# Kernel tuning notes

Measured on AMD Instinct MI355X. Metric: run time of the kernel, lower is better.

Reference implementation:

```python
import jax, jax.numpy as jnp
import numpy as np

N = 204800   # total nodes (4096 subgraphs x 50 nodes)
E = 3276800  # edges (avg degree 16)
B = 4096     # number of subgraphs
IN = 64      # in_feats
HID = 32     # latent_dim per layer
CAT = 128    # 4 * 32 concatenated states
PH = 64      # pooling hidden dim
R = 3        # num_relations
NB = 2       # num_bases
MARGIN = 1.0


def setup_inputs() -> dict:
    key = jax.random.key(0)
    ks = jax.random.split(key, 24)
    s = 0.1
    inp = {}
    inp['x'] = jax.random.normal(ks[0], (N, IN), jnp.float32)
    inp['edge_norm'] = jax.random.uniform(ks[1], (E,), jnp.float32)
    inp['src'] = jax.random.randint(ks[2], (E,), 0, N, jnp.int32)
    inp['dst'] = jax.random.randint(ks[3], (E,), 0, N, jnp.int32)
    inp['etype'] = jax.random.randint(ks[4], (E,), 0, R, jnp.int32)
    inp['graph_id'] = jnp.arange(N, dtype=jnp.int32) // (N // B)
    inp['ntype'] = jax.random.randint(ks[5], (N,), 0, 2, jnp.int32)
    # layer 0: basis-decomposed RelGraphConv (in=64 -> 32)
    inp['bases0'] = jax.random.normal(ks[6], (NB, IN, HID), jnp.float32) * s
    inp['coef0'] = jax.random.normal(ks[7], (R, NB), jnp.float32)
    inp['wself0'] = jax.random.normal(ks[8], (IN, HID), jnp.float32) * s
    inp['bias0'] = jnp.zeros((HID,), jnp.float32)
    # layers 1..3 stacked (32 -> 32 each)
    inp['bases_r'] = jax.random.normal(ks[9], (3, NB, HID, HID), jnp.float32) * s
    inp['coef_r'] = jax.random.normal(ks[10], (3, R, NB), jnp.float32)
    inp['wself_r'] = jax.random.normal(ks[11], (3, HID, HID), jnp.float32) * s
    inp['bias_r'] = jnp.zeros((3, HID), jnp.float32)
    # attention pooling (user / item)
    inp['wp_u'] = jax.random.normal(ks[12], (CAT, PH), jnp.float32) * s
    inp['wt_u'] = jax.random.normal(ks[13], (CAT, PH), jnp.float32) * s
    inp['wp_i'] = jax.random.normal(ks[14], (CAT, PH), jnp.float32) * s
    inp['wt_i'] = jax.random.normal(ks[15], (CAT, PH), jnp.float32) * s
    # MLP head
    inp['w1'] = jax.random.normal(ks[16], (2 * PH, 64), jnp.float32) * s
    inp['b1'] = jnp.zeros((64,), jnp.float32)
    inp['w2'] = jax.random.normal(ks[17], (64, 1), jnp.float32) * s
    inp['b2'] = jnp.zeros((1,), jnp.float32)
    return inp


def _rgcn_layer(h, bases, coef, wself, bias, src, dst, etype, edge_norm):
    # basis decomposition: W_r = sum_b coef[r,b] * bases[b]
    W = jnp.einsum('rb,bio->rio', coef, bases)          # [R, in, out]
    xr = jnp.einsum('ni,rio->nro', h, W)                # [N, R, out] (transform then gather)
    msg = xr[src, etype] * edge_norm[:, None]           # [E, out]
    agg = jax.ops.segment_sum(msg, dst, num_segments=N) # scatter-add to dst
    return jnp.tanh(agg + h @ wself + bias)


def _attn_pool(x, mask, gid, wp, wt):
    # x: [N, CAT], mask: [N] bool (target node type), gid: [N] graph ids
    fmask = mask.astype(x.dtype)
    cnt = jax.ops.segment_sum(fmask, gid, num_segments=B)              # [B]
    tmean = jax.ops.segment_sum(x * fmask[:, None], gid, num_segments=B)
    tmean = tmean / (cnt[:, None] + 1e-8)                              # [B, CAT]
    p = x @ wp                                                          # [N, PH]
    t = tmean @ wt                                                      # [B, PH]
    score = jnp.sum(p * t[gid], axis=-1) / jnp.sqrt(jnp.float32(PH))    # [N]
    score = jnp.where(mask, score, -1e9)
    m = jax.ops.segment_max(score, gid, num_segments=B)                 # [B]
    a = jnp.exp(score - m[gid]) * fmask
    z = jax.ops.segment_sum(a, gid, num_segments=B)
    alpha = a / (z[gid] + 1e-8)
    return jax.ops.segment_sum(alpha[:, None] * p, gid, num_segments=B)  # [B, PH]


def reference(x, edge_norm, src, dst, etype, graph_id, ntype,
              bases0, coef0, wself0, bias0, bases_r, coef_r, wself_r, bias_r,
              wp_u, wt_u, wp_i, wt_i, w1, b1, w2, b2):
    h = x
    states = []
    h = _rgcn_layer(h, bases0, coef0, wself0, bias0, src, dst, etype, edge_norm)
    states.append(h)
    for l in range(3):
        h = _rgcn_layer(h, bases_r[l], coef_r[l], wself_r[l], bias_r[l],
                        src, dst, etype, edge_norm)
        states.append(h)
    hcat = jnp.concatenate(states, axis=1)  # [N, 128]

    mask_u = ntype == 0
    mask_i = ntype == 1

    # triplet contrastive loss over per-graph mean user/item embeddings
    fu = mask_u.astype(hcat.dtype)
    fi = mask_i.astype(hcat.dtype)
    cu = jax.ops.segment_sum(fu, graph_id, num_segments=B) + 1e-8
    ci = jax.ops.segment_sum(fi, graph_id, num_segments=B) + 1e-8
    au = jax.ops.segment_sum(hcat * fu[:, None], graph_id, num_segments=B) / cu[:, None]
    ai = jax.ops.segment_sum(hcat * fi[:, None], graph_id, num_segments=B) / ci[:, None]
    an = jnp.roll(ai, 1, axis=0)  # negatives from shifted graphs
    dpos = jnp.sum((au - ai) ** 2, axis=-1)
    dneg = jnp.sum((au - an) ** 2, axis=-1)
    triplet_loss = jnp.mean(jax.nn.relu(dpos - dneg + MARGIN))

    x_u = _attn_pool(hcat, mask_u, graph_id, wp_u, wt_u)  # [B, 64]
    x_i = _attn_pool(hcat, mask_i, graph_id, wp_i, wt_i)  # [B, 64]
    z = jnp.concatenate([x_u, x_i], axis=1)               # [B, 128]
    z = jax.nn.relu(z @ w1 + b1)                          # dropout off (eval)
    out = jax.nn.sigmoid(z @ w2 + b2)[:, 0]               # [B]
    return out, triplet_loss
```

## Files before the change

kernel.cpp:

```cpp
#include <hip/hip_runtime.h>
#include <cstdint>
#include <cstddef>

#define NN   204800
#define EE   3276800
#define BB   4096
#define GS   50
#define NBUCK 200
#define CHUNK 8192
#define BCAP  17408

typedef __attribute__((ext_vector_type(8))) short short8v;
typedef __attribute__((ext_vector_type(4))) float f32x4;

__device__ __forceinline__ float bf2f(unsigned short u) {
  unsigned int x = ((unsigned int)u) << 16;
  return __int_as_float((int)x);
}
__device__ __forceinline__ unsigned short f2bf(float f) {
  unsigned int x = __float_as_uint(f);
  unsigned int r = (x + 0x7fffu + ((x >> 16) & 1u)) >> 16;
  return (unsigned short)r;
}

__global__ __launch_bounds__(256) void pass1_kernel(const int* __restrict__ src,
                                                    const int* __restrict__ dst,
                                                    const int* __restrict__ etype,
                                                    const float* __restrict__ en,
                                                    int* __restrict__ gcursor,
                                                    int2* __restrict__ staging) {
  __shared__ int2 stage[CHUNK];
  __shared__ unsigned char bid[CHUNK];
  __shared__ int hist[NBUCK], cur[NBUCK], lo[NBUCK], gbase[NBUCK];
  __shared__ int sc[256];
  const int tid = threadIdx.x;
  const int ebase = blockIdx.x * CHUNK;

  for (int i = tid; i < NBUCK; i += 256) hist[i] = 0;
  __syncthreads();
  for (int i = tid; i < CHUNK; i += 256) {
    int bk = dst[ebase + i] >> 10;
    bid[i] = (unsigned char)bk;
    atomicAdd(&hist[bk], 1);
  }
  __syncthreads();
  int hv = (tid < NBUCK) ? hist[tid] : 0;
  sc[tid] = hv;
  __syncthreads();
  for (int off = 1; off < 256; off <<= 1) {
    int t = (tid >= off) ? sc[tid - off] : 0;
    __syncthreads();
    sc[tid] += t;
    __syncthreads();
  }
  if (tid < NBUCK) {
    int excl = sc[tid] - hv;
    lo[tid]  = excl;
    cur[tid] = excl;
    gbase[tid] = hv ? atomicAdd(&gcursor[tid], hv) : 0;
  }
  __syncthreads();
  for (int i = tid; i < CHUNK; i += 256) {
    int bk = bid[i];
    int p = atomicAdd(&cur[bk], 1);
    int s  = src[ebase + i];
    int et = etype[ebase + i];
    int d  = dst[ebase + i];
    int2 r;
    r.x = (s << 12) | (et << 10) | (d & 1023);
    r.y = __float_as_int(en[ebase + i]);
    stage[p] = r;
  }
  __syncthreads();
  const int wave = tid >> 6, lane = tid & 63;
  for (int bk = wave; bk < NBUCK; bk += 4) {
    const int len = hist[bk];
    const int l0  = lo[bk];
    const int gb  = gbase[bk];
    for (int i = lane; i < len; i += 64)
      staging[gb + i] = stage[l0 + i];
  }
}

__global__ __launch_bounds__(256) void pass2_kernel(const int2* __restrict__ staging,
                                                    const int* __restrict__ gcursor,
                                                    int* __restrict__ begs,
                                                    int* __restrict__ ends,
                                                    int2* __restrict__ edata) {
  __shared__ int lhist[1024];
  __shared__ int lcur[1024];
  __shared__ int psum[256];
  const int b = blockIdx.x;
  const int tid = threadIdx.x;
  const int base = b * BCAP;
  const int cnt  = gcursor[b] - base;

  for (int i = tid; i < 1024; i += 256) lhist[i] = 0;
  __syncthreads();
  for (int i = tid; i < cnt; i += 256)
    atomicAdd(&lhist[staging[base + i].x & 1023], 1);
  __syncthreads();
  int s0 = lhist[4 * tid], s1 = lhist[4 * tid + 1];
  int s2 = lhist[4 * tid + 2], s3 = lhist[4 * tid + 3];
  int tot = s0 + s1 + s2 + s3;
  psum[tid] = tot;
  __syncthreads();
  for (int off = 1; off < 256; off <<= 1) {
    int t = (tid >= off) ? psum[tid - off] : 0;
    __syncthreads();
    psum[tid] += t;
    __syncthreads();
  }
  int o0 = base + psum[tid] - tot;
  int o1 = o0 + s0, o2 = o1 + s1, o3 = o2 + s2;
  const int nodeb = b * 1024;
  begs[nodeb + 4 * tid]     = o0;  ends[nodeb + 4 * tid]     = o1;  lcur[4 * tid]     = o0;
  begs[nodeb + 4 * tid + 1] = o1;  ends[nodeb + 4 * tid + 1] = o2;  lcur[4 * tid + 1] = o1;
  begs[nodeb + 4 * tid + 2] = o2;  ends[nodeb + 4 * tid + 2] = o3;  lcur[4 * tid + 2] = o2;
  begs[nodeb + 4 * tid + 3] = o3;  ends[nodeb + 4 * tid + 3] = o3 + s3;  lcur[4 * tid + 3] = o3;
  __syncthreads();
  for (int i = tid; i < cnt; i += 256) {
    int2 r = staging[base + i];
    int pos = atomicAdd(&lcur[r.x & 1023], 1);
    int s  = r.x >> 12;
    int et = (r.x >> 10) & 3;
    int2 outr;
    outr.x = (s << 8) + (et << 6);
    outr.y = r.y;
    edata[pos] = outr;
  }
}

__global__ __launch_bounds__(256) void wprep_kernel(
    const float* __restrict__ bases0, const float* __restrict__ coef0,
    const float* __restrict__ wself0,
    const float* __restrict__ bases_r, const float* __restrict__ coef_r,
    const float* __restrict__ wself_r,
    const float* __restrict__ wp_u, const float* __restrict__ wp_i,
    const float* __restrict__ wt_u, const float* __restrict__ wt_i,
    const float* __restrict__ w1,
    float* __restrict__ Wbuf, int* __restrict__ gcursor) {
  if (blockIdx.x == 0 && threadIdx.x < NBUCK)
    gcursor[threadIdx.x] = threadIdx.x * BCAP;
  int idx = blockIdx.x * 256 + threadIdx.x;
  if (idx < 8192) {
    int i = idx >> 7, j = idx & 127;
    float v;
    if (j < 96) {
      int r = j >> 5, f = j & 31;
      v = coef0[r * 2 + 0] * bases0[0 * 2048 + i * 32 + f]
        + coef0[r * 2 + 1] * bases0[1 * 2048 + i * 32 + f];
    } else {
      v = wself0[i * 32 + (j - 96)];
    }
    Wbuf[idx] = v;
    return;
  }
  int idx2 = idx - 8192;
  if (idx2 < 3 * 4096) {
    int l = idx2 >> 12, rem = idx2 & 4095;
    int i = rem >> 7, j = rem & 127;
    float v;
    if (j < 96) {
      int r = j >> 5, f = j & 31;
      v = coef_r[l * 6 + r * 2 + 0] * bases_r[l * 2048 + 0 * 1024 + i * 32 + f]
        + coef_r[l * 6 + r * 2 + 1] * bases_r[l * 2048 + 1 * 1024 + i * 32 + f];
    } else {
      v = wself_r[l * 1024 + i * 32 + (j - 96)];
    }
    Wbuf[idx] = v;
    return;
  }
  int idx3 = idx2 - 12288;
  if (idx3 < 32768) {
    int side = idx3 >> 14;
    int r = idx3 & 16383;
    int kk = r >> 7, k = r & 127;
    const float* wp = side ? wp_i : wp_u;
    const float* wt = side ? wt_i : wt_u;
    float acc = 0.f;
#pragma unroll 8
    for (int j = 0; j < 64; ++j)
      acc = fmaf(wp[k * 64 + j], wt[kk * 64 + j], acc);
    Wbuf[idx] = acc * 0.125f;
    return;
  }
  int idx4 = idx3 - 32768;
  if (idx4 < 16384) {
    int kp = idx4 >> 6, t = idx4 & 63;
    int side = kp >> 7, k = kp & 127;
    const float* wp = side ? wp_i : wp_u;
    float acc = 0.f;
#pragma unroll 8
    for (int j = 0; j < 64; ++j)
      acc = fmaf(wp[k * 64 + j], w1[(side * 64 + j) * 64 + t], acc);
    Wbuf[idx] = acc;
  }
}

__global__ __launch_bounds__(256) void wprep2_kernel(const float* __restrict__ Wbuf,
                                                     unsigned short* __restrict__ Whi,
                                                     unsigned short* __restrict__ Wlo) {
  int e = blockIdx.x * 256 + threadIdx.x;
  if (e >= 20480) return;
  float v;
  if (e < 8192) {
    int j = e & 7, l = (e >> 3) & 63, c = (e >> 9) & 7, q = e >> 12;
    int k   = q * 32 + (l >> 4) * 8 + j;
    int col = c * 16 + (l & 15);
    v = Wbuf[k * 128 + col];
  } else {
    int e2 = e - 8192;
    int lay = e2 >> 12, r = e2 & 4095;
    int j = r & 7, l = (r >> 3) & 63, qc = r >> 9;
    int q = qc >> 1, c = qc & 1;
    int k = q * 32 + (l >> 4) * 8 + j;
    int o = c * 16 + (l & 15);
    const float* Wc = Wbuf + 8192 + lay * 4096;
    v = (k < 96) ? Wc[(k & 31) * 128 + (k >> 5) * 32 + o]
                 : Wc[(k - 96) * 128 + 96 + o];
  }
  unsigned short hi = f2bf(v);
  Whi[e] = hi;
  Wlo[e] = f2bf(v - bf2f(hi));
}

__global__ __launch_bounds__(256) void transform_l0_kernel(
    const float* __restrict__ x,
    const unsigned short* __restrict__ Whi, const unsigned short* __restrict__ Wlo,
    unsigned short* __restrict__ Tb0) {
  __shared__ float C[64][129];
  const int tid = threadIdx.x;
  const int wv = tid >> 6, l = tid & 63;
  const int l15 = l & 15, kg = l >> 4;
  const int row = blockIdx.x * 64 + wv * 16 + l15;

  short8v ah[2], al[2];
#pragma unroll
  for (int q = 0; q < 2; ++q) {
    const float* xp = x + (size_t)row * 64 + q * 32 + kg * 8;
    const float4 v0 = *reinterpret_cast<const float4*>(xp);
    const float4 v1 = *reinterpret_cast<const float4*>(xp + 4);
    const float vv[8] = {v0.x, v0.y, v0.z, v0.w, v1.x, v1.y, v1.z, v1.w};
#pragma unroll
    for (int f = 0; f < 8; ++f) {
      const unsigned short h = f2bf(vv[f]);
      ah[q][f] = (short)h;
      al[q][f] = (short)f2bf(vv[f] - bf2f(h));
    }
  }

#pragma unroll
  for (int c = 0; c < 8; ++c) {
    f32x4 a = {0.f, 0.f, 0.f, 0.f};
#pragma unroll
    for (int q = 0; q < 2; ++q) {
      const size_t fb = ((size_t)(q * 8 + c) * 64 + l) * 8;
      const short8v bh = *reinterpret_cast<const short8v*>(Whi + fb);
      const short8v bl = *reinterpret_cast<const short8v*>(Wlo + fb);
      a = __builtin_amdgcn_mfma_f32_16x16x32_bf16(ah[q], bh, a, 0, 0, 0);
      a = __builtin_amdgcn_mfma_f32_16x16x32_bf16(al[q], bh, a, 0, 0, 0);
      a = __builtin_amdgcn_mfma_f32_16x16x32_bf16(ah[q], bl, a, 0, 0, 0);
    }
#pragma unroll
    for (int r = 0; r < 4; ++r)
      C[wv * 16 + kg * 4 + r][c * 16 + l15] = a[r];
  }
  __syncthreads();

  const int row64 = tid & 63, q = tid >> 6;
  const int node = blockIdx.x * 64 + row64;
#pragma unroll
  for (int v = 0; v < 4; ++v) {
    const int cb = q * 32 + v * 8;
    uint4 pk;
    pk.x = (unsigned)f2bf(C[row64][cb + 0]) | ((unsigned)f2bf(C[row64][cb + 1]) << 16);
    pk.y = (unsigned)f2bf(C[row64][cb + 2]) | ((unsigned)f2bf(C[row64][cb + 3]) << 16);
    pk.z = (unsigned)f2bf(C[row64][cb + 4]) | ((unsigned)f2bf(C[row64][cb + 5]) << 16);
    pk.w = (unsigned)f2bf(C[row64][cb + 6]) | ((unsigned)f2bf(C[row64][cb + 7]) << 16);
    *reinterpret_cast<uint4*>(Tb0 + (size_t)node * 128 + cb) = pk;
  }
}

__global__ __launch_bounds__(256) void aggregate_l0_kernel(
    const unsigned short* __restrict__ Tb0,
    const int* __restrict__ begs, const int* __restrict__ ends,
    const int2* __restrict__ edata, const float* __restrict__ bias,
    float* __restrict__ hcat, unsigned short* __restrict__ hbA) {
  const int node = blockIdx.x * 32 + (threadIdx.x >> 3);
  const int f4   = (threadIdx.x & 7) * 4;
  const int loff = f4 * 2;
  const char* Tbc = (const char*)Tb0;
  const int beg = begs[node];
  const int end = ends[node];
  const ushort4 sb = *reinterpret_cast<const ushort4*>(Tbc + (size_t)node * 256 + 192 + loff);
  const float4 bv  = *reinterpret_cast<const float4*>(&bias[f4]);
  float ax = bf2f(sb.x) + bv.x, ay = bf2f(sb.y) + bv.y;
  float az = bf2f(sb.z) + bv.z, aw = bf2f(sb.w) + bv.w;

  int k = beg;
  for (; k + 8 <= end; k += 8) {
    int2 ed[8];
#pragma unroll
    for (int u = 0; u < 8; ++u) ed[u] = edata[k + u];
    ushort4 mv[8];
#pragma unroll
    for (int u = 0; u < 8; ++u)
      mv[u] = *reinterpret_cast<const ushort4*>(Tbc + ed[u].x + loff);
#pragma unroll
    for (int u = 0; u < 8; ++u) {
      const float nm = __int_as_float(ed[u].y);
      ax = fmaf(bf2f(mv[u].x), nm, ax);
      ay = fmaf(bf2f(mv[u].y), nm, ay);
      az = fmaf(bf2f(mv[u].z), nm, az);
      aw = fmaf(bf2f(mv[u].w), nm, aw);
    }
  }
  for (; k < end; ++k) {
    int2 e0 = edata[k];
    const float nm = __int_as_float(e0.y);
    ushort4 m0 = *reinterpret_cast<const ushort4*>(Tbc + e0.x + loff);
    ax = fmaf(bf2f(m0.x), nm, ax);
    ay = fmaf(bf2f(m0.y), nm, ay);
    az = fmaf(bf2f(m0.z), nm, az);
    aw = fmaf(bf2f(m0.w), nm, aw);
  }
  float4 o;
  o.x = tanhf(ax); o.y = tanhf(ay); o.z = tanhf(az); o.w = tanhf(aw);
  *reinterpret_cast<float4*>(&hcat[(size_t)node * 128 + f4]) = o;
  ushort4 h;
  h.x = f2bf(o.x); h.y = f2bf(o.y); h.z = f2bf(o.z); h.w = f2bf(o.w);
  *reinterpret_cast<ushort4*>(hbA + (size_t)node * 32 + f4) = h;
}

__global__ __launch_bounds__(256, 8) void agg_tf_kernel(
    const unsigned short* __restrict__ hbX,
    const int* __restrict__ begs, const int* __restrict__ ends,
    const int2* __restrict__ edata,
    const unsigned short* __restrict__ Whi, const unsigned short* __restrict__ Wlo,
    const float* __restrict__ bias,
    float* __restrict__ hcatSlot, unsigned short* __restrict__ hbY) {
  __shared__ __align__(16) unsigned short sld[32][136];
  __shared__ float C[32][33];
  const int tid = threadIdx.x;

  {
    const int nl   = tid >> 3;
    const int node = blockIdx.x * 32 + nl;
    const int f4   = (tid & 7) * 4;
    const int loff = f4 * 2;
    const char* hbc = (const char*)hbX;
    const int beg = begs[node], end = ends[node];
    float a0x = 0.f, a0y = 0.f, a0z = 0.f, a0w = 0.f;
    float a1x = 0.f, a1y = 0.f, a1z = 0.f, a1w = 0.f;
    float a2x = 0.f, a2y = 0.f, a2z = 0.f, a2w = 0.f;

    int k = beg;
    for (; k + 8 <= end; k += 8) {
      int2 ed[8];
#pragma unroll
      for (int u = 0; u < 8; ++u) ed[u] = edata[k + u];
      ushort4 mv[8];
#pragma unroll
      for (int u = 0; u < 8; ++u)
        mv[u] = *reinterpret_cast<const ushort4*>(hbc + ((ed[u].x >> 2) & ~63) + loff);
#pragma unroll
      for (int u = 0; u < 8; ++u) {
        const int et = (ed[u].x >> 6) & 3;
        const float nm = __int_as_float(ed[u].y);
        const float n0 = (et == 0) ? nm : 0.f;
        const float n1 = (et == 1) ? nm : 0.f;
        const float n2 = (et == 2) ? nm : 0.f;
        const float vx = bf2f(mv[u].x), vy = bf2f(mv[u].y);
        const float vz = bf2f(mv[u].z), vw = bf2f(mv[u].w);
        a0x = fmaf(vx, n0, a0x); a0y = fmaf(vy, n0, a0y);
        a0z = fmaf(vz, n0, a0z); a0w = fmaf(vw, n0, a0w);
        a1x = fmaf(vx, n1, a1x); a1y = fmaf(vy, n1, a1y);
        a1z = fmaf(vz, n1, a1z); a1w = fmaf(vw, n1, a1w);
        a2x = fmaf(vx, n2, a2x); a2y = fmaf(vy, n2, a2y);
        a2z = fmaf(vz, n2, a2z); a2w = fmaf(vw, n2, a2w);
      }
    }
    for (; k < end; ++k) {
      int2 e0 = edata[k];
      const int et = (e0.x >> 6) & 3;
      const float nm = __int_as_float(e0.y);
      const float n0 = (et == 0) ? nm : 0.f;
      const float n1 = (et == 1) ? nm : 0.f;
      const float n2 = (et == 2) ? nm : 0.f;
      ushort4 m0 = *reinterpret_cast<const ushort4*>(hbc + ((e0.x >> 2) & ~63) + loff);
      const float vx = bf2f(m0.x), vy = bf2f(m0.y), vz = bf2f(m0.z), vw = bf2f(m0.w);
      a0x = fmaf(vx, n0, a0x); a0y = fmaf(vy, n0, a0y);
      a0z = fmaf(vz, n0, a0z); a0w = fmaf(vw, n0, a0w);
      a1x = fmaf(vx, n1, a1x); a1y = fmaf(vy, n1, a1y);
      a1z = fmaf(vz, n1, a1z); a1w = fmaf(vw, n1, a1w);
      a2x = fmaf(vx, n2, a2x); a2y = fmaf(vy, n2, a2y);
      a2z = fmaf(vz, n2, a2z); a2w = fmaf(vw, n2, a2w);
    }
    ushort4 s0, s1, s2;
    s0.x = f2bf(a0x); s0.y = f2bf(a0y); s0.z = f2bf(a0z); s0.w = f2bf(a0w);
    s1.x = f2bf(a1x); s1.y = f2bf(a1y); s1.z = f2bf(a1z); s1.w = f2bf(a1w);
    s2.x = f2bf(a2x); s2.y = f2bf(a2y); s2.z = f2bf(a2z); s2.w = f2bf(a2w);
    *reinterpret_cast<ushort4*>(&sld[nl][f4])      = s0;
    *reinterpret_cast<ushort4*>(&sld[nl][32 + f4]) = s1;
    *reinterpret_cast<ushort4*>(&sld[nl][64 + f4]) = s2;
    *reinterpret_cast<ushort4*>(&sld[nl][96 + f4]) =
        *reinterpret_cast<const ushort4*>(hbX + (size_t)node * 32 + f4);
  }
  __syncthreads();

  {
    const int w = tid >> 6, l = tid & 63;
    const int rg = w & 1, c = w >> 1;
    const int l15 = l & 15, kg = l >> 4;
    const int row = rg * 16 + l15;
    short8v af[4];
#pragma unroll
    for (int q = 0; q < 4; ++q)
      af[q] = *reinterpret_cast<const short8v*>(&sld[row][q * 32 + kg * 8]);
    f32x4 a = {0.f, 0.f, 0.f, 0.f};
#pragma unroll
    for (int q = 0; q < 4; ++q) {
      const size_t fb = ((size_t)(q * 2 + c) * 64 + l) * 8;
      const short8v bh = *reinterpret_cast<const short8v*>(Whi + fb);
      const short8v bl = *reinterpret_cast<const short8v*>(Wlo + fb);
      a = __builtin_amdgcn_mfma_f32_16x16x32_bf16(af[q], bh, a, 0, 0, 0);
      a = __builtin_amdgcn_mfma_f32_16x16x32_bf16(af[q], bl, a, 0, 0, 0);
    }
#pragma unroll
    for (int r = 0; r < 4; ++r)
      C[rg * 16 + kg * 4 + r][c * 16 + l15] = a[r];
  }
  __syncthreads();

  {
    const int row32 = tid & 31, g = tid >> 5;
    const int node = blockIdx.x * 32 + row32;
    float z[4];
#pragma unroll
    for (int v = 0; v < 4; ++v)
      z[v] = tanhf(C[row32][g * 4 + v] + bias[g * 4 + v]);
    float4 f0 = {z[0], z[1], z[2], z[3]};
    *reinterpret_cast<float4*>(hcatSlot + (size_t)node * 128 + g * 4) = f0;
    if (hbY) {
      ushort4 pk;
      pk.x = f2bf(z[0]); pk.y = f2bf(z[1]); pk.z = f2bf(z[2]); pk.w = f2bf(z[3]);
      *reinterpret_cast<ushort4*>(hbY + (size_t)node * 32 + g * 4) = pk;
    }
  }
}

__global__ __launch_bounds__(256) void pool_head_kernel(
    const float* __restrict__ hcat, const int* __restrict__ ntype,
    const float* __restrict__ Mt,
    const float* __restrict__ W1c,
    const float* __restrict__ b1,
    const float* __restrict__ w2, const float* __restrict__ b2,
    float* __restrict__ out, float* __restrict__ tl) {
  __shared__ float hl[GS * 129];
  __shared__ float scr[1024];
  __shared__ float av2[256];
  __shared__ float red[4];
  __shared__ float cnts[4];
  __shared__ int   snt[64];
  __shared__ int   sntp[64];

  const int g    = (blockIdx.x & 7) * (BB / 8) + (blockIdx.x >> 3);
  const int gp   = (g + BB - 1) & (BB - 1);
  const int tid  = threadIdx.x;
  const int lane = tid & 63;

  const float* hg  = hcat + (size_t)g  * (GS * 128);
  const float* hp  = hcat + (size_t)gp * (GS * 128);
  const int*   ntg = ntype + g  * GS;
  const int*   ntp = ntype + gp * GS;

  if (tid < 64) {
    snt[tid] = (tid < GS) ? ntg[tid] : 99;
    unsigned long long bu = __ballot(snt[tid] == 0);
    unsigned long long bi = __ballot(snt[tid] == 1);
    if (lane == 0) {
      cnts[0] = 1.f / ((float)__popcll(bu) + 1e-8f);
      cnts[1] = 1.f / ((float)__popcll(bi) + 1e-8f);
    }
  } else if (tid < 128) {
    sntp[lane] = (lane < GS) ? ntp[lane] : 99;
    unsigned long long bp = __ballot(sntp[lane] == 1);
    if (lane == 0) cnts[2] = 1.f / ((float)__popcll(bp) + 1e-8f);
  }

  {
    const int rowg = tid >> 5;
    const int kq   = (tid & 31) * 4;
    float spx = 0.f, spy = 0.f, spz = 0.f, spw = 0.f;
#pragma unroll
    for (int p = 0; p < 7; ++p) {
      const int r = rowg + 8 * p;
      if (r < GS) {
        const float4 v = *reinterpret_cast<const float4*>(hg + r * 128 + kq);
        hl[r * 129 + kq + 0] = v.x;
        hl[r * 129 + kq + 1] = v.y;
        hl[r * 129 + kq + 2] = v.z;
        hl[r * 129 + kq + 3] = v.w;
        if (ntp[r] == 1) {
          const float4 w = *reinterpret_cast<const float4*>(hp + r * 128 + kq);
          spx += w.x; spy += w.y; spz += w.z; spw += w.w;
        }
      }
    }
    scr[rowg * 128 + kq + 0] = spx;
    scr[rowg * 128 + kq + 1] = spy;
    scr[rowg * 128 + kq + 2] = spz;
    scr[rowg * 128 + kq + 3] = spw;
  }
  __syncthreads();

  if (tid < 128) {
    const int kf = tid;
    float su = 0.f, si = 0.f;
#pragma unroll
    for (int r = 0; r < GS; ++r) {
      const float v = hl[r * 129 + kf];
      if (snt[r] == 0) su += v; else si += v;
    }
    float sp = 0.f;
#pragma unroll
    for (int rg = 0; rg < 8; ++rg) sp += scr[rg * 128 + kf];
    const float auk = su * cnts[0];
    const float aik = si * cnts[1];
    const float apk = sp * cnts[2];
    av2[kf]       = auk;
    av2[128 + kf] = aik;
    float d1 = (auk - aik) * (auk - aik);
    float d2 = (auk - apk) * (auk - apk);
    for (int o = 32; o; o >>= 1) {
      d1 += __shfl_xor(d1, o);
      d2 += __shfl_xor(d2, o);
    }
    if (lane == 0) { red[tid >> 6] = d1; red[2 + (tid >> 6)] = d2; }
  }
  __syncthreads();

  {
    const int side = tid >> 7, kf = tid & 127;
    const float* M  = Mt + (size_t)side * 16384 + kf;
    const float* av = av2 + side * 128;
    float a0 = 0.f, a1 = 0.f, a2 = 0.f, a3 = 0.f;
#pragma unroll 4
    for (int kk = 0; kk < 128; kk += 4) {
      a0 = fmaf(M[(kk + 0) * 128], av[kk + 0], a0);
      a1 = fmaf(M[(kk + 1) * 128], av[kk + 1], a1);
      a2 = fmaf(M[(kk + 2) * 128], av[kk + 2], a2);
      a3 = fmaf(M[(kk + 3) * 128], av[kk + 3], a3);
    }
    scr[tid] = (a0 + a1) + (a2 + a3);
  }
  if (tid == 0) tl[g] = fmaxf(0.f, (red[0] + red[1]) - (red[2] + red[3]) + 1.0f);
  __syncthreads();

  if (tid < 128) {
    const int side = tid >> 6;
    const float* q = scr + side * 128;
    float v = -1e9f;
    bool msk = false;
    if (lane < GS) {
      msk = (snt[lane] == side);
      float a0 = 0.f, a1 = 0.f;
#pragma unroll 8
      for (int k = 0; k < 128; k += 2) {
        a0 = fmaf(hl[lane * 129 + k], q[k], a0);
        a1 = fmaf(hl[lane * 129 + k + 1], q[k + 1], a1);
      }
      v = msk ? (a0 + a1) : -1e9f;
    }
    float m = v;
    for (int o = 32; o; o >>= 1) m = fmaxf(m, __shfl_xor(m, o));
    float e = (lane < GS && msk) ? expf(v - m) : 0.f;
    float z = e;
    for (int o = 32; o; o >>= 1) z += __shfl_xor(z, o);
    const float invz = 1.f / (z + 1e-8f);
    if (lane < GS) scr[256 + side * 64 + lane] = e * invz;
  }
  __syncthreads();

  {
    const int side = tid >> 7, kf = tid & 127;
    const float* a = scr + 256 + side * 64;
    float acc = 0.f;
#pragma unroll
    for (int nl = 0; nl < GS; ++nl)
      acc = fmaf(a[nl], hl[nl * 129 + kf], acc);
    scr[384 + side * 128 + kf] = acc;
  }
  __syncthreads();

  {
    const int j = tid & 63, c = tid >> 6;
    const float* Wc = W1c + (size_t)c * 64 * 64 + j;
    const float* cv = scr + 384 + c * 64;
    float a0 = 0.f, a1 = 0.f, a2 = 0.f, a3 = 0.f;
#pragma unroll 4
    for (int k = 0; k < 64; k += 4) {
      a0 = fmaf(Wc[(k + 0) * 64], cv[k + 0], a0);
      a1 = fmaf(Wc[(k + 1) * 64], cv[k + 1], a1);
      a2 = fmaf(Wc[(k + 2) * 64], cv[k + 2], a2);
      a3 = fmaf(Wc[(k + 3) * 64], cv[k + 3], a3);
    }
    scr[640 + c * 64 + j] = (a0 + a1) + (a2 + a3);
  }
  __syncthreads();

  if (tid < 64) {
    const float z1 = fmaxf(b1[tid] + scr[640 + tid] + scr[704 + tid] +
                           scr[768 + tid] + scr[832 + tid], 0.f);
    float p = z1 * w2[tid];
    for (int o = 32; o; o >>= 1) p += __shfl_xor(p, o);
    if (tid == 0) out[g] = 1.f / (1.f + expf(-(p + b2[0])));
  }
}

__global__ __launch_bounds__(256) void tl_reduce_kernel(const float* __restrict__ tl,
                                                        float* __restrict__ out) {
  __shared__ float s[256];
  float acc = 0.f;
  for (int i = threadIdx.x; i < BB; i += 256) acc += tl[i];
  s[threadIdx.x] = acc;
  __syncthreads();
  for (int off = 128; off > 0; off >>= 1) {
    if (threadIdx.x < off) s[threadIdx.x] += s[threadIdx.x + off];
    __syncthreads();
  }
  if (threadIdx.x == 0) out[BB] = s[0] * (1.f / (float)BB);
}

extern "C" void kernel_launch(void* const* d_in, const int* in_sizes, int n_in,
                              void* d_out, int out_size, void* d_ws, size_t ws_size,
                              hipStream_t stream) {
  const float* x        = (const float*)d_in[0];
  const float* edge_nrm = (const float*)d_in[1];
  const int*   src      = (const int*)d_in[2];
  const int*   dst      = (const int*)d_in[3];
  const int*   etype    = (const int*)d_in[4];
  const int*   ntype    = (const int*)d_in[6];
  const float* bases0   = (const float*)d_in[7];
  const float* coef0    = (const float*)d_in[8];
  const float* wself0   = (const float*)d_in[9];
  const float* bias0    = (const float*)d_in[10];
  const float* bases_r  = (const float*)d_in[11];
  const float* coef_r   = (const float*)d_in[12];
  const float* wself_r  = (const float*)d_in[13];
  const float* bias_r   = (const float*)d_in[14];
  const float* wp_u     = (const float*)d_in[15];
  const float* wt_u     = (const float*)d_in[16];
  const float* wp_i     = (const float*)d_in[17];
  const float* wt_i     = (const float*)d_in[18];
  const float* w1       = (const float*)d_in[19];
  const float* b1       = (const float*)d_in[20];
  const float* w2       = (const float*)d_in[21];
  const float* b2       = (const float*)d_in[22];
  float* out = (float*)d_out;

  float*          hcat = (float*)d_ws;
  float*          R    = hcat + (size_t)NN * 128;
  int2*           staging = (int2*)R;
  unsigned short* Tb0  = (unsigned short*)R;
  unsigned short* hbA  = Tb0 + (size_t)NN * 128;
  unsigned short* hbB  = hbA + (size_t)NN * 32;
  int2*  edata   = (int2*)(R + (size_t)NN * 128);
  int*   begs    = (int*)(edata + (size_t)NBUCK * BCAP);
  int*   ends    = begs + NN;
  int*   gcursor = ends + NN;
  float* Wbuf    = (float*)(gcursor + 256);
  unsigned short* Whi = (unsigned short*)(Wbuf + 69632);
  unsigned short* Wlo = Whi + 20480;
  float* tl      = Wbuf + 69632 + 10240;

  size_t need = ((size_t)NN * 128 * 2 + (size_t)NBUCK * BCAP * 2 + 2 * NN + 256 +
                 69632 + 10240 + BB) * 4;
  if (ws_size < need) return;

  wprep_kernel<<<(69632 + 255) / 256, 256, 0, stream>>>(
      bases0, coef0, wself0, bases_r, coef_r, wself_r,
      wp_u, wp_i, wt_u, wt_i, w1, Wbuf, gcursor);
  wprep2_kernel<<<80, 256, 0, stream>>>(Wbuf, Whi, Wlo);

  pass1_kernel<<<EE / CHUNK, 256, 0, stream>>>(src, dst, etype, edge_nrm,
                                               gcursor, staging);
  pass2_kernel<<<NBUCK, 256, 0, stream>>>(staging, gcursor, begs, ends, edata);

  transform_l0_kernel<<<NN / 64, 256, 0, stream>>>(x, Whi, Wlo, Tb0);
  aggregate_l0_kernel<<<NN / 32, 256, 0, stream>>>(Tb0, begs, ends, edata,
                                                   bias0, hcat, hbA);

  agg_tf_kernel<<<NN / 32, 256, 0, stream>>>(
      hbA, begs, ends, edata, Whi + 8192, Wlo + 8192, bias_r,
      hcat + 32, hbB);
  agg_tf_kernel<<<NN / 32, 256, 0, stream>>>(
      hbB, begs, ends, edata, Whi + 12288, Wlo + 12288, bias_r + 32,
      hcat + 64, hbA);
  agg_tf_kernel<<<NN / 32, 256, 0, stream>>>(
      hbA, begs, ends, edata, Whi + 16384, Wlo + 16384, bias_r + 64,
      hcat + 96, nullptr);

  pool_head_kernel<<<BB, 256, 0, stream>>>(hcat, ntype,
                                           Wbuf + 20480, Wbuf + 53248,
                                           b1, w2, b2, out, tl);
  tl_reduce_kernel<<<1, 256, 0, stream>>>(tl, out);
}
```

Before: 501.9 us.

## Fuse layer-0 transform with edge bucketing; split edge data into offsets and bf16 norms

Merges the layer-0 dense transform and the first edge-bucketing pass into one launch, interleaving blocks (one bucketing block per nine) with a shared-memory union, so the GEMM work can overlap the scatter. The staging buffer moves into the hcat region so it no longer aliases Tb0. Per-edge records become a separate int offset array plus a bf16 norm array read with nontemporal loads, cutting edge-stream bytes from 8 to 6 per edge across four aggregation passes. Storing norms in bf16 loses precision in the edge weights.

Result: slower. 621.2 us (+23.8%).

```diff
diff --git a/kernel.cpp b/kernel.cpp
--- a/kernel.cpp
+++ b/kernel.cpp
@@ -9,6 +9,7 @@
 #define NBUCK 200
 #define CHUNK 8192
 #define BCAP  17408
+#define ESLOTS ((size_t)NBUCK * BCAP)
 
 typedef __attribute__((ext_vector_type(8))) short short8v;
 typedef __attribute__((ext_vector_type(4))) float f32x4;
@@ -23,62 +24,124 @@
   return (unsigned short)r;
 }
 
-__global__ __launch_bounds__(256) void pass1_kernel(const int* __restrict__ src,
-                                                    const int* __restrict__ dst,
-                                                    const int* __restrict__ etype,
-                                                    const float* __restrict__ en,
-                                                    int* __restrict__ gcursor,
-                                                    int2* __restrict__ staging) {
-  __shared__ int2 stage[CHUNK];
-  __shared__ unsigned char bid[CHUNK];
-  __shared__ int hist[NBUCK], cur[NBUCK], lo[NBUCK], gbase[NBUCK];
-  __shared__ int sc[256];
+struct P1Sh {
+  int2 stage[CHUNK];
+  unsigned char bid[CHUNK];
+  int hist[NBUCK], cur[NBUCK], lo[NBUCK], gbase[NBUCK];
+  int sc[256];
+};
+struct TfSh { float C[64][129]; };
+
+__global__ __launch_bounds__(256) void fused_tp1_kernel(
+    const float* __restrict__ x,
+    const unsigned short* __restrict__ Whi, const unsigned short* __restrict__ Wlo,
+    unsigned short* __restrict__ Tb0,
+    const int* __restrict__ src, const int* __restrict__ dst,
+    const int* __restrict__ etype, const float* __restrict__ en,
+    int* __restrict__ gcursor, int2* __restrict__ staging) {
+  __shared__ union { P1Sh p1; TfSh tf; } sh;
   const int tid = threadIdx.x;
-  const int ebase = blockIdx.x * CHUNK;
-
-  for (int i = tid; i < NBUCK; i += 256) hist[i] = 0;
+
+  if (blockIdx.x % 9 != 0) {
+    const int tb = blockIdx.x - blockIdx.x / 9 - 1;
+    const int wv = tid >> 6, l = tid & 63;
+    const int l15 = l & 15, kg = l >> 4;
+    const int row = tb * 64 + wv * 16 + l15;
+
+    short8v ah[2], al[2];
+#pragma unroll
+    for (int q = 0; q < 2; ++q) {
+      const float* xp = x + (size_t)row * 64 + q * 32 + kg * 8;
+      const float4 v0 = *reinterpret_cast<const float4*>(xp);
+      const float4 v1 = *reinterpret_cast<const float4*>(xp + 4);
+      const float vv[8] = {v0.x, v0.y, v0.z, v0.w, v1.x, v1.y, v1.z, v1.w};
+#pragma unroll
+      for (int f = 0; f < 8; ++f) {
+        const unsigned short h = f2bf(vv[f]);
+        ah[q][f] = (short)h;
+        al[q][f] = (short)f2bf(vv[f] - bf2f(h));
+      }
+    }
+
+#pragma unroll
+    for (int c = 0; c < 8; ++c) {
+      f32x4 a = {0.f, 0.f, 0.f, 0.f};
+#pragma unroll
+      for (int q = 0; q < 2; ++q) {
+        const size_t fb = ((size_t)(q * 8 + c) * 64 + l) * 8;
+        const short8v bh = *reinterpret_cast<const short8v*>(Whi + fb);
+        const short8v bl = *reinterpret_cast<const short8v*>(Wlo + fb);
+        a = __builtin_amdgcn_mfma_f32_16x16x32_bf16(ah[q], bh, a, 0, 0, 0);
+        a = __builtin_amdgcn_mfma_f32_16x16x32_bf16(al[q], bh, a, 0, 0, 0);
+        a = __builtin_amdgcn_mfma_f32_16x16x32_bf16(ah[q], bl, a, 0, 0, 0);
+      }
+#pragma unroll
+      for (int r = 0; r < 4; ++r)
+        sh.tf.C[wv * 16 + kg * 4 + r][c * 16 + l15] = a[r];
+    }
+    __syncthreads();
+
+    const int row64 = tid & 63, q = tid >> 6;
+    const int node = tb * 64 + row64;
+#pragma unroll
+    for (int v = 0; v < 4; ++v) {
+      const int cb = q * 32 + v * 8;
+      uint4 pk;
+      pk.x = (unsigned)f2bf(sh.tf.C[row64][cb + 0]) | ((unsigned)f2bf(sh.tf.C[row64][cb + 1]) << 16);
+      pk.y = (unsigned)f2bf(sh.tf.C[row64][cb + 2]) | ((unsigned)f2bf(sh.tf.C[row64][cb + 3]) << 16);
+      pk.z = (unsigned)f2bf(sh.tf.C[row64][cb + 4]) | ((unsigned)f2bf(sh.tf.C[row64][cb + 5]) << 16);
+      pk.w = (unsigned)f2bf(sh.tf.C[row64][cb + 6]) | ((unsigned)f2bf(sh.tf.C[row64][cb + 7]) << 16);
+      *reinterpret_cast<uint4*>(Tb0 + (size_t)node * 128 + cb) = pk;
+    }
+    return;
+  }
+
+  const int pb = blockIdx.x / 9;
+  const int ebase = pb * CHUNK;
+
+  for (int i = tid; i < NBUCK; i += 256) sh.p1.hist[i] = 0;
   __syncthreads();
   for (int i = tid; i < CHUNK; i += 256) {
     int bk = dst[ebase + i] >> 10;
-    bid[i] = (unsigned char)bk;
-    atomicAdd(&hist[bk], 1);
-  }
-  __syncthreads();
-  int hv = (tid < NBUCK) ? hist[tid] : 0;
-  sc[tid] = hv;
+    sh.p1.bid[i] = (unsigned char)bk;
+    atomicAdd(&sh.p1.hist[bk], 1);
+  }
+  __syncthreads();
+  int hv = (tid < NBUCK) ? sh.p1.hist[tid] : 0;
+  sh.p1.sc[tid] = hv;
   __syncthreads();
   for (int off = 1; off < 256; off <<= 1) {
-    int t = (tid >= off) ? sc[tid - off] : 0;
+    int t = (tid >= off) ? sh.p1.sc[tid - off] : 0;
     __syncthreads();
-    sc[tid] += t;
+    sh.p1.sc[tid] += t;
     __syncthreads();
   }
   if (tid < NBUCK) {
-    int excl = sc[tid] - hv;
-    lo[tid]  = excl;
-    cur[tid] = excl;
-    gbase[tid] = hv ? atomicAdd(&gcursor[tid], hv) : 0;
+    int excl = sh.p1.sc[tid] - hv;
+    sh.p1.lo[tid]  = excl;
+    sh.p1.cur[tid] = excl;
+    sh.p1.gbase[tid] = hv ? atomicAdd(&gcursor[tid], hv) : 0;
   }
   __syncthreads();
   for (int i = tid; i < CHUNK; i += 256) {
-    int bk = bid[i];
-    int p = atomicAdd(&cur[bk], 1);
+    int bk = sh.p1.bid[i];
+    int p = atomicAdd(&sh.p1.cur[bk], 1);
     int s  = src[ebase + i];
     int et = etype[ebase + i];
     int d  = dst[ebase + i];
     int2 r;
     r.x = (s << 12) | (et << 10) | (d & 1023);
     r.y = __float_as_int(en[ebase + i]);
-    stage[p] = r;
+    sh.p1.stage[p] = r;
   }
   __syncthreads();
   const int wave = tid >> 6, lane = tid & 63;
   for (int bk = wave; bk < NBUCK; bk += 4) {
-    const int len = hist[bk];
-    const int l0  = lo[bk];
-    const int gb  = gbase[bk];
+    const int len = sh.p1.hist[bk];
+    const int l0  = sh.p1.lo[bk];
+    const int gb  = sh.p1.gbase[bk];
     for (int i = lane; i < len; i += 64)
-      staging[gb + i] = stage[l0 + i];
+      staging[gb + i] = sh.p1.stage[l0 + i];
   }
 }
 
@@ -86,7 +149,8 @@
                                                     const int* __restrict__ gcursor,
                                                     int* __restrict__ begs,
                                                     int* __restrict__ ends,
-                                                    int2* __restrict__ edata) {
+                                                    int* __restrict__ offs,
+                                                    unsigned short* __restrict__ norms) {
   __shared__ int lhist[1024];
   __shared__ int lcur[1024];
   __shared__ int psum[256];
@@ -124,10 +188,8 @@
     int pos = atomicAdd(&lcur[r.x & 1023], 1);
     int s  = r.x >> 12;
     int et = (r.x >> 10) & 3;
-    int2 outr;
-    outr.x = (s << 8) + (et << 6);
-    outr.y = r.y;
-    edata[pos] = outr;
+    offs[pos]  = (s << 8) + (et << 6);
+    norms[pos] = f2bf(__int_as_float(r.y));
   }
 }
 
@@ -225,67 +287,11 @@
   Wlo[e] = f2bf(v - bf2f(hi));
 }
 
-__global__ __launch_bounds__(256) void transform_l0_kernel(
-    const float* __restrict__ x,
-    const unsigned short* __restrict__ Whi, const unsigned short* __restrict__ Wlo,
-    unsigned short* __restrict__ Tb0) {
-  __shared__ float C[64][129];
-  const int tid = threadIdx.x;
-  const int wv = tid >> 6, l = tid & 63;
-  const int l15 = l & 15, kg = l >> 4;
-  const int row = blockIdx.x * 64 + wv * 16 + l15;
-
-  short8v ah[2], al[2];
-#pragma unroll
-  for (int q = 0; q < 2; ++q) {
-    const float* xp = x + (size_t)row * 64 + q * 32 + kg * 8;
-    const float4 v0 = *reinterpret_cast<const float4*>(xp);
-    const float4 v1 = *reinterpret_cast<const float4*>(xp + 4);
-    const float vv[8] = {v0.x, v0.y, v0.z, v0.w, v1.x, v1.y, v1.z, v1.w};
-#pragma unroll
-    for (int f = 0; f < 8; ++f) {
-      const unsigned short h = f2bf(vv[f]);
-      ah[q][f] = (short)h;
-      al[q][f] = (short)f2bf(vv[f] - bf2f(h));
-    }
-  }
-
-#pragma unroll
-  for (int c = 0; c < 8; ++c) {
-    f32x4 a = {0.f, 0.f, 0.f, 0.f};
-#pragma unroll
-    for (int q = 0; q < 2; ++q) {
-      const size_t fb = ((size_t)(q * 8 + c) * 64 + l) * 8;
-      const short8v bh = *reinterpret_cast<const short8v*>(Whi + fb);
-      const short8v bl = *reinterpret_cast<const short8v*>(Wlo + fb);
-      a = __builtin_amdgcn_mfma_f32_16x16x32_bf16(ah[q], bh, a, 0, 0, 0);
-      a = __builtin_amdgcn_mfma_f32_16x16x32_bf16(al[q], bh, a, 0, 0, 0);
-      a = __builtin_amdgcn_mfma_f32_16x16x32_bf16(ah[q], bl, a, 0, 0, 0);
-    }
-#pragma unroll
-    for (int r = 0; r < 4; ++r)
-      C[wv * 16 + kg * 4 + r][c * 16 + l15] = a[r];
-  }
-  __syncthreads();
-
-  const int row64 = tid & 63, q = tid >> 6;
-  const int node = blockIdx.x * 64 + row64;
-#pragma unroll
-  for (int v = 0; v < 4; ++v) {
-    const int cb = q * 32 + v * 8;
-    uint4 pk;
-    pk.x = (unsigned)f2bf(C[row64][cb + 0]) | ((unsigned)f2bf(C[row64][cb + 1]) << 16);
-    pk.y = (unsigned)f2bf(C[row64][cb + 2]) | ((unsigned)f2bf(C[row64][cb + 3]) << 16);
-    pk.z = (unsigned)f2bf(C[row64][cb + 4]) | ((unsigned)f2bf(C[row64][cb + 5]) << 16);
-    pk.w = (unsigned)f2bf(C[row64][cb + 6]) | ((unsigned)f2bf(C[row64][cb + 7]) << 16);
-    *reinterpret_cast<uint4*>(Tb0 + (size_t)node * 128 + cb) = pk;
-  }
-}
-
 __global__ __launch_bounds__(256) void aggregate_l0_kernel(
     const unsigned short* __restrict__ Tb0,
     const int* __restrict__ begs, const int* __restrict__ ends,
-    const int2* __restrict__ edata, const float* __restrict__ bias,
+    const int* __restrict__ offs, const unsigned short* __restrict__ norms,
+    const float* __restrict__ bias,
     float* __restrict__ hcat, unsigned short* __restrict__ hbA) {
   const int node = blockIdx.x * 32 + (threadIdx.x >> 3);
   const int f4   = (threadIdx.x & 7) * 4;
@@ -300,16 +306,18 @@
 
   int k = beg;
   for (; k + 8 <= end; k += 8) {
-    int2 ed[8];
-#pragma unroll
-    for (int u = 0; u < 8; ++u) ed[u] = edata[k + u];
+    int od[8]; unsigned short nb[8];
+#pragma unroll
+    for (int u = 0; u < 8; ++u) od[u] = __builtin_nontemporal_load(offs + k + u);
+#pragma unroll
+    for (int u = 0; u < 8; ++u) nb[u] = __builtin_nontemporal_load(norms + k + u);
     ushort4 mv[8];
 #pragma unroll
     for (int u = 0; u < 8; ++u)
-      mv[u] = *reinterpret_cast<const ushort4*>(Tbc + ed[u].x + loff);
+      mv[u] = *reinterpret_cast<const ushort4*>(Tbc + od[u] + loff);
 #pragma unroll
     for (int u = 0; u < 8; ++u) {
-      const float nm = __int_as_float(ed[u].y);
+      const float nm = bf2f(nb[u]);
       ax = fmaf(bf2f(mv[u].x), nm, ax);
       ay = fmaf(bf2f(mv[u].y), nm, ay);
       az = fmaf(bf2f(mv[u].z), nm, az);
@@ -317,9 +325,9 @@
     }
   }
   for (; k < end; ++k) {
-    int2 e0 = edata[k];
-    const float nm = __int_as_float(e0.y);
-    ushort4 m0 = *reinterpret_cast<const ushort4*>(Tbc + e0.x + loff);
+    const int od = offs[k];
+    const float nm = bf2f(norms[k]);
+    ushort4 m0 = *reinterpret_cast<const ushort4*>(Tbc + od + loff);
     ax = fmaf(bf2f(m0.x), nm, ax);
     ay = fmaf(bf2f(m0.y), nm, ay);
     az = fmaf(bf2f(m0.z), nm, az);
@@ -336,7 +344,7 @@
 __global__ __launch_bounds__(256, 8) void agg_tf_kernel(
     const unsigned short* __restrict__ hbX,
     const int* __restrict__ begs, const int* __restrict__ ends,
-    const int2* __restrict__ edata,
+    const int* __restrict__ offs, const unsigned short* __restrict__ norms,
     const unsigned short* __restrict__ Whi, const unsigned short* __restrict__ Wlo,
     const float* __restrict__ bias,
     float* __restrict__ hcatSlot, unsigned short* __restrict__ hbY) {
@@ -357,17 +365,19 @@
 
     int k = beg;
     for (; k + 8 <= end; k += 8) {
-      int2 ed[8];
-#pragma unroll
-      for (int u = 0; u < 8; ++u) ed[u] = edata[k + u];
+      int od[8]; unsigned short nb[8];
+#pragma unroll
+      for (int u = 0; u < 8; ++u) od[u] = __builtin_nontemporal_load(offs + k + u);
+#pragma unroll
+      for (int u = 0; u < 8; ++u) nb[u] = __builtin_nontemporal_load(norms + k + u);
       ushort4 mv[8];
 #pragma unroll
       for (int u = 0; u < 8; ++u)
-        mv[u] = *reinterpret_cast<const ushort4*>(hbc + ((ed[u].x >> 2) & ~63) + loff);
+        mv[u] = *reinterpret_cast<const ushort4*>(hbc + ((od[u] >> 2) & ~63) + loff);
 #pragma unroll
       for (int u = 0; u < 8; ++u) {
-        const int et = (ed[u].x >> 6) & 3;
-        const float nm = __int_as_float(ed[u].y);
+        const int et = (od[u] >> 6) & 3;
+        const float nm = bf2f(nb[u]);
         const float n0 = (et == 0) ? nm : 0.f;
         const float n1 = (et == 1) ? nm : 0.f;
         const float n2 = (et == 2) ? nm : 0.f;
@@ -382,13 +392,13 @@
       }
     }
     for (; k < end; ++k) {
-      int2 e0 = edata[k];
-      const int et = (e0.x >> 6) & 3;
-      const float nm = __int_as_float(e0.y);
+      const int od = offs[k];
+      const int et = (od >> 6) & 3;
+      const float nm = bf2f(norms[k]);
       const float n0 = (et == 0) ? nm : 0.f;
       const float n1 = (et == 1) ? nm : 0.f;
       const float n2 = (et == 2) ? nm : 0.f;
-      ushort4 m0 = *reinterpret_cast<const ushort4*>(hbc + ((e0.x >> 2) & ~63) + loff);
+      ushort4 m0 = *reinterpret_cast<const ushort4*>(hbc + ((od >> 2) & ~63) + loff);
       const float vx = bf2f(m0.x), vy = bf2f(m0.y), vz = bf2f(m0.z), vw = bf2f(m0.w);
       a0x = fmaf(vx, n0, a0x); a0y = fmaf(vy, n0, a0y);
       a0z = fmaf(vz, n0, a0z); a0w = fmaf(vw, n0, a0w);
@@ -661,13 +671,14 @@
   float* out = (float*)d_out;
 
   float*          hcat = (float*)d_ws;
+  int2*           staging = (int2*)hcat;
   float*          R    = hcat + (size_t)NN * 128;
-  int2*           staging = (int2*)R;
   unsigned short* Tb0  = (unsigned short*)R;
   unsigned short* hbA  = Tb0 + (size_t)NN * 128;
   unsigned short* hbB  = hbA + (size_t)NN * 32;
-  int2*  edata   = (int2*)(R + (size_t)NN * 128);
-  int*   begs    = (int*)(edata + (size_t)NBUCK * BCAP);
+  int*            offs = (int*)(R + (size_t)NN * 128);
+  unsigned short* norms= (unsigned short*)(offs + ESLOTS);
+  int*   begs    = (int*)(norms + ESLOTS);
   int*   ends    = begs + NN;
   int*   gcursor = ends + NN;
   float* Wbuf    = (float*)(gcursor + 256);
@@ -675,8 +686,8 @@
   unsigned short* Wlo = Whi + 20480;
   float* tl      = Wbuf + 69632 + 10240;
 
-  size_t need = ((size_t)NN * 128 * 2 + (size_t)NBUCK * BCAP * 2 + 2 * NN + 256 +
-                 69632 + 10240 + BB) * 4;
+  size_t need = ((size_t)NN * 128 * 2 + ESLOTS + ESLOTS / 2 + 2 * NN +
+                 256 + 69632 + 10240 + BB) * 4;
   if (ws_size < need) return;
 
   wprep_kernel<<<(69632 + 255) / 256, 256, 0, stream>>>(
@@ -684,22 +695,22 @@
       wp_u, wp_i, wt_u, wt_i, w1, Wbuf, gcursor);
   wprep2_kernel<<<80, 256, 0, stream>>>(Wbuf, Whi, Wlo);
 
-  pass1_kernel<<<EE / CHUNK, 256, 0, stream>>>(src, dst, etype, edge_nrm,
-                                               gcursor, staging);
-  pass2_kernel<<<NBUCK, 256, 0, stream>>>(staging, gcursor, begs, ends, edata);
-
-  transform_l0_kernel<<<NN / 64, 256, 0, stream>>>(x, Whi, Wlo, Tb0);
-  aggregate_l0_kernel<<<NN / 32, 256, 0, stream>>>(Tb0, begs, ends, edata,
+  fused_tp1_kernel<<<NN / 64 + EE / CHUNK, 256, 0, stream>>>(
+      x, Whi, Wlo, Tb0, src, dst, etype, edge_nrm, gcursor, staging);
+  pass2_kernel<<<NBUCK, 256, 0, stream>>>(staging, gcursor, begs, ends,
+                                          offs, norms);
+
+  aggregate_l0_kernel<<<NN / 32, 256, 0, stream>>>(Tb0, begs, ends, offs, norms,
                                                    bias0, hcat, hbA);
 
   agg_tf_kernel<<<NN / 32, 256, 0, stream>>>(
-      hbA, begs, ends, edata, Whi + 8192, Wlo + 8192, bias_r,
+      hbA, begs, ends, offs, norms, Whi + 8192, Wlo + 8192, bias_r,
       hcat + 32, hbB);
   agg_tf_kernel<<<NN / 32, 256, 0, stream>>>(
-      hbB, begs, ends, edata, Whi + 12288, Wlo + 12288, bias_r + 32,
+      hbB, begs, ends, offs, norms, Whi + 12288, Wlo + 12288, bias_r + 32,
       hcat + 64, hbA);
   agg_tf_kernel<<<NN / 32, 256, 0, stream>>>(
-      hbA, begs, ends, edata, Whi + 16384, Wlo + 16384, bias_r + 64,
+      hbA, begs, ends, offs, norms, Whi + 16384, Wlo + 16384, bias_r + 64,
       hcat + 96, nullptr);
 
   pool_head_kernel<<<BB, 256, 0, stream>>>(hcat, ntype,
```
